# Kernel tuning notes

Hardware: AMD Instinct MI355X
Metric: run time of the kernel (lower is better)

## Reference

```python
import jax, jax.numpy as jnp
import numpy as np

# norse.LIFCell default parameters
DT = 1e-3
TAU_SYN_INV = 200.0   # 1 / 5e-3
TAU_MEM_INV = 100.0   # 1 / 1e-2
V_TH = 1.0
V_LEAK = 0.0
V_RESET = 0.0
ALPHA = 100.0         # SuperSpike surrogate slope

T, B, N_IN, N_HIDDEN, N_OUT = 16, 4096, 784, 256, 10


@jax.custom_vjp
def heaviside(x):
    return (x > 0).astype(x.dtype)

def _h_fwd(x):
    return heaviside(x), x

def _h_bwd(x, g):
    # SuperSpike surrogate: d/dx H(x) ~ 1 / (alpha*|x| + 1)^2
    return (g / (ALPHA * jnp.abs(x) + 1.0) ** 2,)

heaviside.defvjp(_h_fwd, _h_bwd)


def lif_step(inp, v, i):
    """One norse lif_step: Euler-integrate v and i, spike, hard reset."""
    v_decayed = v + DT * TAU_MEM_INV * ((V_LEAK - v) + i)
    i_decayed = i - DT * TAU_SYN_INV * i
    z = heaviside(v_decayed - V_TH)
    v_new = (1.0 - z) * v_decayed + z * V_RESET
    i_new = i_decayed + inp
    return z, v_new, i_new


def setup_inputs() -> dict:
    key = jax.random.key(0)
    k1, k2, k3, k4, k5 = jax.random.split(key, 5)
    # binary spike trains (T, B, N_IN)
    spike_input = (jax.random.uniform(k1, (T, B, N_IN)) < 0.3).astype(jnp.float32)
    lim1 = float(1.0 / np.sqrt(N_IN))
    lim2 = float(1.0 / np.sqrt(N_HIDDEN))
    W1 = jax.random.uniform(k2, (N_HIDDEN, N_IN), minval=-lim1, maxval=lim1, dtype=jnp.float32)
    b1 = jax.random.uniform(k3, (N_HIDDEN,), minval=-lim1, maxval=lim1, dtype=jnp.float32)
    W2 = jax.random.uniform(k4, (N_OUT, N_HIDDEN), minval=-lim2, maxval=lim2, dtype=jnp.float32)
    b2 = jax.random.uniform(k5, (N_OUT,), minval=-lim2, maxval=lim2, dtype=jnp.float32)
    return {"spike_input": spike_input, "W1": W1, "b1": b1, "W2": W2, "b2": b2}


def reference(spike_input, W1, b1, W2, b2):
    batch = spike_input.shape[1]
    nh, no = W1.shape[0], W2.shape[0]
    dtype = spike_input.dtype
    # LIFCell with state=None starts at v=v_leak, i=0
    init = (jnp.full((batch, nh), V_LEAK, dtype), jnp.zeros((batch, nh), dtype),
            jnp.full((batch, no), V_LEAK, dtype), jnp.zeros((batch, no), dtype))

    def step(carry, x_t):
        v1, i1, v2, i2 = carry
        c1 = x_t @ W1.T + b1                 # (B, N_HIDDEN)
        z1, v1, i1 = lif_step(c1, v1, i1)
        c2 = z1 @ W2.T + b2                  # (B, N_OUT)
        z2, v2, i2 = lif_step(c2, v2, i2)
        return (v1, i1, v2, i2), z2

    _, zs = jax.lax.scan(step, init, spike_input)  # zs: (T, B, N_OUT)
    return zs.sum(axis=0)                          # (B, N_OUT)
```

## Files before the change

kernel.cpp:

```cpp
#include <hip/hip_runtime.h>


#define T_STEPS 16
#define B_SZ    4096
#define N_IN    784
#define N_HID   256
#define N_OUT   10
#define M_TOT   (T_STEPS * B_SZ)
#define KPAD    800
#define NT      25

typedef __bf16 bf16x8 __attribute__((ext_vector_type(8)));
typedef float  f32x4  __attribute__((ext_vector_type(4)));
typedef unsigned short ushort_t;
typedef unsigned int   u32;

#define GLOAD_LDS(SRC, DST) \
    __builtin_amdgcn_global_load_lds( \
        (const __attribute__((address_space(1))) void*)(SRC), \
        (__attribute__((address_space(3))) void*)(DST), 16, 0, 0)

__device__ __forceinline__ unsigned short bf16_rne(float f) {
    u32 u = __builtin_bit_cast(u32, f);
    u += 0x7fffu + ((u >> 16) & 1u);
    return (unsigned short)(u >> 16);
}

__global__ __launch_bounds__(256) void conv_w(
    const float* __restrict__ W1,
    ushort_t* __restrict__ Whi, ushort_t* __restrict__ Wlo)
{
    const int idx = blockIdx.x * 256 + threadIdx.x;
    if (idx >= N_HID * KPAD) return;
    const int n = idx / KPAD, k = idx % KPAD;
    unsigned short hh = 0, ll = 0;
    if (k < N_IN) {
        const float wv = W1[n * N_IN + k];
        hh = bf16_rne(wv);
        const float hf = __builtin_bit_cast(float, (u32)hh << 16);
        ll = bf16_rne(wv - hf);
    }
    Whi[idx] = hh;
    Wlo[idx] = ll;
}

__device__ __forceinline__ u32 pack_hi16(u32 a, u32 b) {
    return (a >> 16) | (b & 0xffff0000u);
}

__global__ __launch_bounds__(512, 2) void gemm1_mfma(
    const float* __restrict__ X,
    const ushort_t* __restrict__ Whi,
    const ushort_t* __restrict__ Wlo,
    const float* __restrict__ b1,
    float* __restrict__ C)
{
    __shared__ float    Afs[2][128 * 32];
    __shared__ ushort_t Bhs[2][256 * 32];
    __shared__ ushort_t Bls[2][256 * 32];

    const int tid  = threadIdx.x;
    const int lane = tid & 63;
    const int w    = tid >> 6;
    const int wm   = w >> 2;
    const int wn   = w & 3;
    const int m0   = blockIdx.x * 128;
    const int ls   = lane >> 4;
    const int lr   = lane & 15;

    f32x4 acc[4][4];
    #pragma unroll
    for (int i = 0; i < 4; ++i)
        #pragma unroll
        for (int j = 0; j < 4; ++j)
            #pragma unroll
            for (int q = 0; q < 4; ++q)
                acc[i][j][q] = 0.0f;

    auto stage = [&](int bi, int k0) {
        #pragma unroll
        for (int q = 0; q < 2; ++q) {
            const int u   = q * 512 + tid;
            const int row = u >> 3;
            const int ks  = ((u & 7) ^ (row & 7)) << 2;
            const int kk  = (k0 + ks < N_IN) ? (k0 + ks) : 0;
            GLOAD_LDS(X + (size_t)(m0 + row) * N_IN + kk, &Afs[bi][u * 4]);
        }
        #pragma unroll
        for (int q = 0; q < 2; ++q) {
            const int u   = q * 512 + tid;
            const int row = u >> 2;
            const int sl  = ((u & 3) ^ ((row >> 1) & 3)) << 3;
            const size_t so = (size_t)row * KPAD + k0 + sl;
            GLOAD_LDS(Whi + so, &Bhs[bi][u * 8]);
            GLOAD_LDS(Wlo + so, &Bls[bi][u * 8]);
        }
    };

    int aOff0[4], aOff1[4], bOff[4];
    #pragma unroll
    for (int i = 0; i < 4; ++i) {
        const int R = wm * 64 + i * 16 + lr;
        aOff0[i] = R * 32 + ((((2 * ls)     ^ (R & 7))) << 2);
        aOff1[i] = R * 32 + ((((2 * ls + 1) ^ (R & 7))) << 2);
    }
    #pragma unroll
    for (int j = 0; j < 4; ++j) {
        const int R = wn * 64 + j * 16 + lr;
        bOff[j] = R * 32 + ((ls ^ ((R >> 1) & 3)) << 3);
    }

    stage(0, 0);
    stage(1, 32);

    for (int kt = 0; kt < NT; ++kt) {
        const int buf = kt & 1;

        asm volatile("s_waitcnt vmcnt(6)" ::: "memory");
        __builtin_amdgcn_sched_barrier(0);
        __builtin_amdgcn_s_barrier();
        __builtin_amdgcn_sched_barrier(0);

        bf16x8 af[4], bh[4], bl[4];
        #pragma unroll
        for (int i = 0; i < 4; ++i) {
            const float4 fa = *reinterpret_cast<const float4*>(&Afs[buf][aOff0[i]]);
            const float4 fb = *reinterpret_cast<const float4*>(&Afs[buf][aOff1[i]]);
            uint4 pk;
            pk.x = pack_hi16(__builtin_bit_cast(u32, fa.x), __builtin_bit_cast(u32, fa.y));
            pk.y = pack_hi16(__builtin_bit_cast(u32, fa.z), __builtin_bit_cast(u32, fa.w));
            pk.z = pack_hi16(__builtin_bit_cast(u32, fb.x), __builtin_bit_cast(u32, fb.y));
            pk.w = pack_hi16(__builtin_bit_cast(u32, fb.z), __builtin_bit_cast(u32, fb.w));
            af[i] = __builtin_bit_cast(bf16x8, pk);
        }
        #pragma unroll
        for (int j = 0; j < 4; ++j) {
            bh[j] = *reinterpret_cast<const bf16x8*>(&Bhs[buf][bOff[j]]);
            bl[j] = *reinterpret_cast<const bf16x8*>(&Bls[buf][bOff[j]]);
        }

        asm volatile("s_waitcnt lgkmcnt(0)" ::: "memory");
        __builtin_amdgcn_sched_barrier(0);
        __builtin_amdgcn_s_barrier();
        __builtin_amdgcn_sched_barrier(0);

        stage(buf, (kt + 2 < NT) ? (kt + 2) * 32 : 0);

        __builtin_amdgcn_s_setprio(1);
        #pragma unroll
        for (int i = 0; i < 4; ++i)
            #pragma unroll
            for (int j = 0; j < 4; ++j)
                acc[i][j] = __builtin_amdgcn_mfma_f32_16x16x32_bf16(
                    af[i], bh[j], acc[i][j], 0, 0, 0);
        #pragma unroll
        for (int i = 0; i < 4; ++i)
            #pragma unroll
            for (int j = 0; j < 4; ++j)
                acc[i][j] = __builtin_amdgcn_mfma_f32_16x16x32_bf16(
                    af[i], bl[j], acc[i][j], 0, 0, 0);
        __builtin_amdgcn_s_setprio(0);
    }

    #pragma unroll
    for (int j = 0; j < 4; ++j) {
        const int col  = wn * 64 + j * 16 + lr;
        const float bb = b1[col];
        #pragma unroll
        for (int i = 0; i < 4; ++i) {
            const int rbase = m0 + wm * 64 + i * 16 + (ls << 2);
            #pragma unroll
            for (int q = 0; q < 4; ++q)
                C[(size_t)(rbase + q) * N_HID + col] = acc[i][j][q] + bb;
        }
    }
}

__global__ __launch_bounds__(256) void lif1_kernel(float* __restrict__ C1)
{
    const int g = blockIdx.x * 256 + threadIdx.x;
    const size_t stride = (size_t)B_SZ * N_HID;
    float v = 0.0f, cur = 0.0f;
    #pragma unroll
    for (int t = 0; t < T_STEPS; ++t) {
        const size_t off = (size_t)t * stride + g;
        const float c = C1[off];
        const float vd = v + 0.1f * ((0.0f - v) + cur);
        const float id = cur - 0.2f * cur;
        const bool  sp = vd > 1.0f;
        C1[off] = sp ? 1.0f : 0.0f;
        v = sp ? 0.0f : vd;
        cur = id + c;
    }
}

__global__ __launch_bounds__(640) void gemm2_f32(
    const float* __restrict__ Z, const float* __restrict__ W2,
    const float* __restrict__ b2, float* __restrict__ C2)
{
    __shared__ float zs[64 * 268];
    __shared__ float ws[N_OUT * N_HID];
    const int tid = threadIdx.x;
    const int m0 = blockIdx.x * 64;

    for (int idx = tid; idx < 4096; idx += 640) {
        const int r = idx >> 6;
        const int c = (idx & 63) << 2;
        *(float4*)&zs[r * 268 + c] =
            *(const float4*)&Z[(size_t)(m0 + r) * N_HID + c];
    }
    *(float4*)&ws[tid * 4] = *(const float4*)&W2[tid * 4];
    __syncthreads();

    const int o = tid >> 6;
    const int r = tid & 63;
    float acc = b2[o];
    #pragma unroll
    for (int k = 0; k < N_HID; k += 4) {
        const float4 z4 = *(const float4*)&zs[r * 268 + k];
        const float4 w4 = *(const float4*)&ws[o * N_HID + k];
        acc += z4.x * w4.x + z4.y * w4.y + z4.z * w4.z + z4.w * w4.w;
    }
    C2[(size_t)(m0 + r) * N_OUT + o] = acc;
}

__global__ __launch_bounds__(256) void lif2_kernel(
    const float* __restrict__ C2, float* __restrict__ out)
{
    const int g = blockIdx.x * 256 + threadIdx.x;
    const int stride = B_SZ * N_OUT;
    float v = 0.0f, cur = 0.0f, s = 0.0f;
    #pragma unroll
    for (int t = 0; t < T_STEPS; ++t) {
        const float c = C2[t * stride + g];
        const float vd = v + 0.1f * ((0.0f - v) + cur);
        const float id = cur - 0.2f * cur;
        const bool  sp = vd > 1.0f;
        s += sp ? 1.0f : 0.0f;
        v = sp ? 0.0f : vd;
        cur = id + c;
    }
    out[g] = s;
}

extern "C" void kernel_launch(void* const* d_in, const int* in_sizes, int n_in,
                              void* d_out, int out_size, void* d_ws, size_t ws_size,
                              hipStream_t stream)
{
    const float* X  = (const float*)d_in[0];
    const float* W1 = (const float*)d_in[1];
    const float* b1 = (const float*)d_in[2];
    const float* W2 = (const float*)d_in[3];
    const float* b2 = (const float*)d_in[4];
    float* out = (float*)d_out;

    ushort_t* Whi = (ushort_t*)d_ws;
    ushort_t* Wlo = Whi + N_HID * KPAD;
    float* C1 = (float*)((char*)d_ws + (1 << 20));
    float* C2 = C1 + (size_t)M_TOT * N_HID;

    conv_w<<<(N_HID * KPAD + 255) / 256, 256, 0, stream>>>(W1, Whi, Wlo);

    gemm1_mfma<<<M_TOT / 128, 512, 0, stream>>>(X, Whi, Wlo, b1, C1);

    lif1_kernel<<<(B_SZ * N_HID) / 256, 256, 0, stream>>>(C1);

    gemm2_f32<<<M_TOT / 64, 640, 0, stream>>>(C1, W2, b2, C2);

    lif2_kernel<<<(B_SZ * N_OUT) / 256, 256, 0, stream>>>(C2, out);
}
```

Baseline: 151.4 us.

## Split gemm1 into 128x128 tiles with single-buffered LDS and XCD-aware block remap

The GEMM1 tile changes from 128x256 per 512-thread block to 128x128 per 256-thread block, which doubles the grid and splits the N dimension across two blocks. A block-index remap groups blocks by XCD so the two N-halves of the same M rows can share the X tile in cache. LDS double buffering and the manual waitcnt/setprio scheduling are replaced with a single buffer and __syncthreads. The aim is more resident blocks per CU and better L2 reuse. The cost is that each X tile is now read twice and loads no longer overlap compute within a block.

```diff
diff --git a/kernel.cpp b/kernel.cpp
--- a/kernel.cpp
+++ b/kernel.cpp
@@ -48,25 +48,28 @@
     return (a >> 16) | (b & 0xffff0000u);
 }
 
-__global__ __launch_bounds__(512, 2) void gemm1_mfma(
+__global__ __launch_bounds__(256, 3) void gemm1_mfma(
     const float* __restrict__ X,
     const ushort_t* __restrict__ Whi,
     const ushort_t* __restrict__ Wlo,
     const float* __restrict__ b1,
     float* __restrict__ C)
 {
-    __shared__ float    Afs[2][128 * 32];
-    __shared__ ushort_t Bhs[2][256 * 32];
-    __shared__ ushort_t Bls[2][256 * 32];
+    __shared__ float    Afs[128 * 32];
+    __shared__ ushort_t Bhs[128 * 32];
+    __shared__ ushort_t Bls[128 * 32];
 
     const int tid  = threadIdx.x;
     const int lane = tid & 63;
     const int w    = tid >> 6;
-    const int wm   = w >> 2;
-    const int wn   = w & 3;
-    const int m0   = blockIdx.x * 128;
-    const int ls   = lane >> 4;
-    const int lr   = lane & 15;
+    const int wm   = w >> 1;
+    const int wn   = w & 1;
+    const int bid = blockIdx.x;
+    const int lb  = (bid & 7) * 128 + (bid >> 3);
+    const int m0  = (lb >> 1) * 128;
+    const int n0  = (lb & 1) * 128;
+    const int ls  = lane >> 4;
+    const int lr  = lane & 15;
 
     f32x4 acc[4][4];
     #pragma unroll
@@ -77,23 +80,23 @@
             for (int q = 0; q < 4; ++q)
                 acc[i][j][q] = 0.0f;
 
-    auto stage = [&](int bi, int k0) {
-        #pragma unroll
-        for (int q = 0; q < 2; ++q) {
-            const int u   = q * 512 + tid;
+    auto stage = [&](int k0) {
+        #pragma unroll
+        for (int q = 0; q < 4; ++q) {
+            const int u   = q * 256 + tid;
             const int row = u >> 3;
             const int ks  = ((u & 7) ^ (row & 7)) << 2;
             const int kk  = (k0 + ks < N_IN) ? (k0 + ks) : 0;
-            GLOAD_LDS(X + (size_t)(m0 + row) * N_IN + kk, &Afs[bi][u * 4]);
+            GLOAD_LDS(X + (size_t)(m0 + row) * N_IN + kk, &Afs[u * 4]);
         }
         #pragma unroll
         for (int q = 0; q < 2; ++q) {
-            const int u   = q * 512 + tid;
+            const int u   = q * 256 + tid;
             const int row = u >> 2;
             const int sl  = ((u & 3) ^ ((row >> 1) & 3)) << 3;
-            const size_t so = (size_t)row * KPAD + k0 + sl;
-            GLOAD_LDS(Whi + so, &Bhs[bi][u * 8]);
-            GLOAD_LDS(Wlo + so, &Bls[bi][u * 8]);
+            const size_t so = (size_t)(n0 + row) * KPAD + k0 + sl;
+            GLOAD_LDS(Whi + so, &Bhs[u * 8]);
+            GLOAD_LDS(Wlo + so, &Bls[u * 8]);
         }
     };
 
@@ -110,22 +113,16 @@
         bOff[j] = R * 32 + ((ls ^ ((R >> 1) & 3)) << 3);
     }
 
-    stage(0, 0);
-    stage(1, 32);
+    stage(0);
 
     for (int kt = 0; kt < NT; ++kt) {
-        const int buf = kt & 1;
-
-        asm volatile("s_waitcnt vmcnt(6)" ::: "memory");
-        __builtin_amdgcn_sched_barrier(0);
-        __builtin_amdgcn_s_barrier();
-        __builtin_amdgcn_sched_barrier(0);
+        __syncthreads();
 
         bf16x8 af[4], bh[4], bl[4];
         #pragma unroll
         for (int i = 0; i < 4; ++i) {
-            const float4 fa = *reinterpret_cast<const float4*>(&Afs[buf][aOff0[i]]);
-            const float4 fb = *reinterpret_cast<const float4*>(&Afs[buf][aOff1[i]]);
+            const float4 fa = *reinterpret_cast<const float4*>(&Afs[aOff0[i]]);
+            const float4 fb = *reinterpret_cast<const float4*>(&Afs[aOff1[i]]);
             uint4 pk;
             pk.x = pack_hi16(__builtin_bit_cast(u32, fa.x), __builtin_bit_cast(u32, fa.y));
             pk.y = pack_hi16(__builtin_bit_cast(u32, fa.z), __builtin_bit_cast(u32, fa.w));
@@ -135,18 +132,14 @@
         }
         #pragma unroll
         for (int j = 0; j < 4; ++j) {
-            bh[j] = *reinterpret_cast<const bf16x8*>(&Bhs[buf][bOff[j]]);
-            bl[j] = *reinterpret_cast<const bf16x8*>(&Bls[buf][bOff[j]]);
-        }
-
-        asm volatile("s_waitcnt lgkmcnt(0)" ::: "memory");
-        __builtin_amdgcn_sched_barrier(0);
-        __builtin_amdgcn_s_barrier();
-        __builtin_amdgcn_sched_barrier(0);
-
-        stage(buf, (kt + 2 < NT) ? (kt + 2) * 32 : 0);
-
-        __builtin_amdgcn_s_setprio(1);
+            bh[j] = *reinterpret_cast<const bf16x8*>(&Bhs[bOff[j]]);
+            bl[j] = *reinterpret_cast<const bf16x8*>(&Bls[bOff[j]]);
+        }
+
+        __syncthreads();
+
+        if (kt + 1 < NT) stage((kt + 1) * 32);
+
         #pragma unroll
         for (int i = 0; i < 4; ++i)
             #pragma unroll
@@ -159,12 +152,11 @@
             for (int j = 0; j < 4; ++j)
                 acc[i][j] = __builtin_amdgcn_mfma_f32_16x16x32_bf16(
                     af[i], bl[j], acc[i][j], 0, 0, 0);
-        __builtin_amdgcn_s_setprio(0);
     }
 
     #pragma unroll
     for (int j = 0; j < 4; ++j) {
-        const int col  = wn * 64 + j * 16 + lr;
+        const int col  = n0 + wn * 64 + j * 16 + lr;
         const float bb = b1[col];
         #pragma unroll
         for (int i = 0; i < 4; ++i) {
@@ -261,7 +253,7 @@
 
     conv_w<<<(N_HID * KPAD + 255) / 256, 256, 0, stream>>>(W1, Whi, Wlo);
 
-    gemm1_mfma<<<M_TOT / 128, 512, 0, stream>>>(X, Whi, Wlo, b1, C1);
+    gemm1_mfma<<<M_TOT / 128 * (N_HID / 128), 256, 0, stream>>>(X, Whi, Wlo, b1, C1);
 
     lif1_kernel<<<(B_SZ * N_HID) / 256, 256, 0, stream>>>(C1);
 
```

Measured after the change: 139.9 us. -7.5%, faster.
